# Performance work log

Hardware: AMD Instinct MI355X
Metric: run time of the kernel (lower is better)

Reference implementation:

```python
import jax, jax.numpy as jnp
import numpy as np

B, N, IN_C, HID_C, OUT_C = 64, 1024, 16, 64, 32


def process_graph(graph):
    # graph: [B, N, N]; add self-loops, then row-normalize by inverse degree.
    n = graph.shape[-1]
    g = graph + jnp.eye(n, dtype=graph.dtype)
    deg = jnp.sum(g, axis=-1)                      # [B, N]
    inv_deg = jnp.where(deg == 0, jnp.zeros_like(deg), 1.0 / deg)
    # diag(inv_deg) @ g == row-wise broadcast scale (avoids O(N^3) diag matmul)
    return g * inv_deg[..., None]                  # [B, N, N]


def setup_inputs() -> dict:
    key = jax.random.key(0)
    kx, kg, k1, kb1, k2, kb2 = jax.random.split(key, 6)
    x = jax.random.normal(kx, (B, N, IN_C), dtype=jnp.float32)
    graph = jax.random.uniform(kg, (B, N, N), dtype=jnp.float32)
    # nn.Linear default init: U(-1/sqrt(fan_in), 1/sqrt(fan_in))
    lim1 = 1.0 / np.sqrt(IN_C)
    W1 = jax.random.uniform(k1, (HID_C, IN_C), minval=-lim1, maxval=lim1, dtype=jnp.float32)
    b1 = jax.random.uniform(kb1, (HID_C,), minval=-lim1, maxval=lim1, dtype=jnp.float32)
    lim2 = 1.0 / np.sqrt(HID_C)
    W2 = jax.random.uniform(k2, (OUT_C, HID_C), minval=-lim2, maxval=lim2, dtype=jnp.float32)
    b2 = jax.random.uniform(kb2, (OUT_C,), minval=-lim2, maxval=lim2, dtype=jnp.float32)
    return {"x": x, "graph": graph, "W1": W1, "b1": b1, "W2": W2, "b2": b2}


def reference(x, graph, W1, b1, W2, b2):
    g = process_graph(graph)                                   # [B, N, N]
    h = jnp.einsum('bnc,hc->bnh', x, W1) + b1                  # linear_1
    h = jax.nn.relu(jnp.einsum('bnm,bmh->bnh', g, h))          # propagate + ReLU
    o = jnp.einsum('bnh,oh->bno', h, W2) + b2                  # linear_2
    o = jax.nn.relu(jnp.einsum('bnm,bmo->bno', g, o))          # propagate + ReLU
    return o                                                   # [B, N, OUT_C]
```

## Files before the change

### kernel.cpp

```cpp
#include <hip/hip_runtime.h>

typedef __attribute__((ext_vector_type(8))) short s16x8;
typedef __attribute__((ext_vector_type(8))) unsigned short u16x8;
typedef __attribute__((ext_vector_type(4))) float f32x4;

#define B_   64
#define N_   1024
#define CIN_ 16
#define CH_  64
#define CO_  32

__device__ __forceinline__ unsigned short f2bf(float f){
  unsigned int u = __float_as_uint(f);
  u += 0x7fffu + ((u >> 16) & 1u);
  return (unsigned short)(u >> 16);
}

__global__ __launch_bounds__(256) void k_linear1(
    const float* __restrict__ x, const float* __restrict__ W1,
    const float* __restrict__ b1, unsigned short* __restrict__ H1T){
  int gt   = blockIdx.x * 256 + threadIdx.x;
  int wave = gt >> 6;
  int lane = gt & 63;
  int b    = wave >> 4;
  int nl0  = (wave & 15) << 6;

  const f32x4* xv = (const f32x4*)(x + ((size_t)(b * N_ + nl0 + lane)) * CIN_);
  float xr[16];
#pragma unroll
  for (int i = 0; i < 4; ++i){
    f32x4 v = xv[i];
#pragma unroll
    for (int e = 0; e < 4; ++e) xr[i*4+e] = v[e];
  }
  for (int h = 0; h < CH_; ++h){
    float acc = b1[h];
#pragma unroll
    for (int c = 0; c < CIN_; ++c) acc += xr[c] * W1[h * CIN_ + c];
    H1T[((size_t)(b * CH_ + h)) * N_ + nl0 + lane] = f2bf(acc);
  }
}

__global__ __launch_bounds__(256) void k_prop1(
    const float* __restrict__ graph, const unsigned short* __restrict__ H1T,
    const float* __restrict__ W2, const float* __restrict__ b2,
    unsigned short* __restrict__ O1T){
  __shared__ unsigned short sH2[4][16 * 64];

  const int b    = blockIdx.x >> 4;
  const int m0   = (blockIdx.x & 15) << 6;
  const int tid  = threadIdx.x;
  const int w    = tid >> 6, lane = tid & 63;
  const int l15  = lane & 15, lk = lane >> 4;
  const int gn   = m0 + (w << 4) + l15;
  const int ksd  = (m0 + (w << 4)) >> 5;

  const float* gA = graph + ((size_t)b << 20) + ((size_t)gn << 10) + (lk << 3);
  const unsigned short* hB = H1T + (size_t)(b * CH_ + l15) * N_ + (lk << 3);

  f32x4 acc[4] = {{0,0,0,0},{0,0,0,0},{0,0,0,0},{0,0,0,0}};
  float deg = 0.f;

  f32x4 a0 = __builtin_nontemporal_load((const f32x4*)(gA));
  f32x4 a1 = __builtin_nontemporal_load((const f32x4*)(gA + 4));
  u16x8 b0 = *(const u16x8*)(hB);
  u16x8 b1f = *(const u16x8*)(hB + 16 * N_);
  u16x8 b2f = *(const u16x8*)(hB + 32 * N_);
  u16x8 b3f = *(const u16x8*)(hB + 48 * N_);

  for (int ks = 0; ks < 32; ++ks){
    const int kn = (((ks + 1) & 31) << 5);
    f32x4 na0 = __builtin_nontemporal_load((const f32x4*)(gA + kn));
    f32x4 na1 = __builtin_nontemporal_load((const f32x4*)(gA + kn + 4));
    u16x8 nb0 = *(const u16x8*)(hB + kn);
    u16x8 nb1 = *(const u16x8*)(hB + 16 * N_ + kn);
    u16x8 nb2 = *(const u16x8*)(hB + 32 * N_ + kn);
    u16x8 nb3 = *(const u16x8*)(hB + 48 * N_ + kn);

    float va[8] = {a0[0], a0[1], a0[2], a0[3], a1[0], a1[1], a1[2], a1[3]};
    if (ks == ksd){
      const int d0 = (ks << 5) + (lk << 3);
#pragma unroll
      for (int e = 0; e < 8; ++e) va[e] += (d0 + e == gn) ? 1.f : 0.f;
    }
#pragma unroll
    for (int e = 0; e < 8; ++e) deg += va[e];
    s16x8 af;
#pragma unroll
    for (int e = 0; e < 8; ++e) af[e] = (short)f2bf(va[e]);

    acc[0] = __builtin_amdgcn_mfma_f32_16x16x32_bf16(af, (s16x8)b0,  acc[0], 0, 0, 0);
    acc[1] = __builtin_amdgcn_mfma_f32_16x16x32_bf16(af, (s16x8)b1f, acc[1], 0, 0, 0);
    acc[2] = __builtin_amdgcn_mfma_f32_16x16x32_bf16(af, (s16x8)b2f, acc[2], 0, 0, 0);
    acc[3] = __builtin_amdgcn_mfma_f32_16x16x32_bf16(af, (s16x8)b3f, acc[3], 0, 0, 0);

    a0 = na0; a1 = na1; b0 = nb0; b1f = nb1; b2f = nb2; b3f = nb3;
  }

  deg += __shfl_xor(deg, 16);
  deg += __shfl_xor(deg, 32);
  float ideg = 1.f / deg;
  float idv[4];
#pragma unroll
  for (int j = 0; j < 4; ++j) idv[j] = __shfl(ideg, (lk << 2) + j);

#pragma unroll
  for (int cf = 0; cf < 4; ++cf){
#pragma unroll
    for (int j = 0; j < 4; ++j){
      float hv = acc[cf][j] * idv[j];
      hv = hv > 0.f ? hv : 0.f;
      int row = (lk << 2) + j;
      int col = (cf << 4) + l15;
      sH2[w][(row << 6) + (col ^ ((row & 7) << 3))] = f2bf(hv);
    }
  }
  __syncthreads();
  s16x8 a2[2];
#pragma unroll
  for (int kk = 0; kk < 2; ++kk)
    a2[kk] = *(const s16x8*)&sH2[w][(l15 << 6) + (((kk << 5) + (lk << 3)) ^ ((l15 & 7) << 3))];

  f32x4 acc2[2] = {{0,0,0,0},{0,0,0,0}};
#pragma unroll
  for (int kk = 0; kk < 2; ++kk){
#pragma unroll
    for (int cf = 0; cf < 2; ++cf){
      const f32x4* wp = (const f32x4*)(W2 + ((cf << 4) + l15) * CH_ + (kk << 5) + (lk << 3));
      f32x4 w0 = wp[0], w1 = wp[1];
      s16x8 bw;
#pragma unroll
      for (int e = 0; e < 4; ++e){ bw[e] = (short)f2bf(w0[e]); bw[4 + e] = (short)f2bf(w1[e]); }
      acc2[cf] = __builtin_amdgcn_mfma_f32_16x16x32_bf16(a2[kk], bw, acc2[cf], 0, 0, 0);
    }
  }
#pragma unroll
  for (int cf = 0; cf < 2; ++cf){
    float badd = b2[(cf << 4) + l15];
#pragma unroll
    for (int j = 0; j < 4; ++j){
      float v = acc2[cf][j] + badd;
      int n = m0 + (w << 4) + (lk << 2) + j;
      O1T[((size_t)(b * CO_ + (cf << 4) + l15)) * N_ + n] = f2bf(v);
    }
  }
}

__global__ __launch_bounds__(256) void k_prop2(
    const float* __restrict__ graph, const unsigned short* __restrict__ O1T,
    float* __restrict__ out){
  const int b    = blockIdx.x >> 4;
  const int m0   = (blockIdx.x & 15) << 6;
  const int tid  = threadIdx.x;
  const int w    = tid >> 6, lane = tid & 63;
  const int l15  = lane & 15, lk = lane >> 4;
  const int gn   = m0 + (w << 4) + l15;
  const int ksd  = (m0 + (w << 4)) >> 5;

  const float* gA = graph + ((size_t)b << 20) + ((size_t)gn << 10) + (lk << 3);
  const unsigned short* oB = O1T + (size_t)(b * CO_ + l15) * N_ + (lk << 3);

  f32x4 acc[2] = {{0,0,0,0},{0,0,0,0}};
  float deg = 0.f;

  f32x4 a0 = __builtin_nontemporal_load((const f32x4*)(gA));
  f32x4 a1 = __builtin_nontemporal_load((const f32x4*)(gA + 4));
  u16x8 b0 = *(const u16x8*)(oB);
  u16x8 b1f = *(const u16x8*)(oB + 16 * N_);

  for (int ks = 0; ks < 32; ++ks){
    const int kn = (((ks + 1) & 31) << 5);
    f32x4 na0 = __builtin_nontemporal_load((const f32x4*)(gA + kn));
    f32x4 na1 = __builtin_nontemporal_load((const f32x4*)(gA + kn + 4));
    u16x8 nb0 = *(const u16x8*)(oB + kn);
    u16x8 nb1 = *(const u16x8*)(oB + 16 * N_ + kn);

    float va[8] = {a0[0], a0[1], a0[2], a0[3], a1[0], a1[1], a1[2], a1[3]};
    if (ks == ksd){
      const int d0 = (ks << 5) + (lk << 3);
#pragma unroll
      for (int e = 0; e < 8; ++e) va[e] += (d0 + e == gn) ? 1.f : 0.f;
    }
#pragma unroll
    for (int e = 0; e < 8; ++e) deg += va[e];
    s16x8 af;
#pragma unroll
    for (int e = 0; e < 8; ++e) af[e] = (short)f2bf(va[e]);

    acc[0] = __builtin_amdgcn_mfma_f32_16x16x32_bf16(af, (s16x8)b0,  acc[0], 0, 0, 0);
    acc[1] = __builtin_amdgcn_mfma_f32_16x16x32_bf16(af, (s16x8)b1f, acc[1], 0, 0, 0);

    a0 = na0; a1 = na1; b0 = nb0; b1f = nb1;
  }

  deg += __shfl_xor(deg, 16);
  deg += __shfl_xor(deg, 32);
  float ideg = 1.f / deg;
  float idv[4];
#pragma unroll
  for (int j = 0; j < 4; ++j) idv[j] = __shfl(ideg, (lk << 2) + j);

#pragma unroll
  for (int cf = 0; cf < 2; ++cf){
#pragma unroll
    for (int j = 0; j < 4; ++j){
      float v = acc[cf][j] * idv[j];
      v = v > 0.f ? v : 0.f;
      int n = m0 + (w << 4) + (lk << 2) + j;
      out[((size_t)(b * N_ + n)) * CO_ + (cf << 4) + l15] = v;
    }
  }
}

extern "C" void kernel_launch(void* const* d_in, const int* in_sizes, int n_in,
                              void* d_out, int out_size, void* d_ws, size_t ws_size,
                              hipStream_t stream){
  (void)in_sizes; (void)n_in; (void)out_size; (void)ws_size;
  const float* x     = (const float*)d_in[0];
  const float* graph = (const float*)d_in[1];
  const float* W1    = (const float*)d_in[2];
  const float* b1    = (const float*)d_in[3];
  const float* W2    = (const float*)d_in[4];
  const float* b2    = (const float*)d_in[5];
  float* out = (float*)d_out;

  unsigned short* H1T = (unsigned short*)d_ws;
  unsigned short* O1T = (unsigned short*)((char*)d_ws + ((size_t)8 << 20));

  k_linear1<<<256, 256, 0, stream>>>(x, W1, b1, H1T);
  k_prop1<<<B_ * 16, 256, 0, stream>>>(graph, H1T, W2, b2, O1T);
  k_prop2<<<B_ * 16, 256, 0, stream>>>(graph, O1T, out);
}
```

Before: 526.5 us.

## Cache bf16 graph and inverse degrees in prop1 for reuse in prop2

The first propagation kernel now writes the bf16-converted graph tile (self-loop included) and the per-row inverse degree to workspace. The second propagation kernel reads this half-size bf16 graph instead of re-reading the fp32 graph, and loads the precomputed inverse degree instead of recomputing it. This is meant to cut the dominant graph traffic in prop2 from 256MB to 128MB. The cost is an extra 128MB write in prop1, a two-deep register prefetch with a reversed k loop in prop2, and reliance on workspace being large enough (about 144MB).

```diff
diff --git a/kernel.cpp b/kernel.cpp
--- a/kernel.cpp
+++ b/kernel.cpp
@@ -44,7 +44,8 @@
 __global__ __launch_bounds__(256) void k_prop1(
     const float* __restrict__ graph, const unsigned short* __restrict__ H1T,
     const float* __restrict__ W2, const float* __restrict__ b2,
-    unsigned short* __restrict__ O1T){
+    unsigned short* __restrict__ O1T, unsigned short* __restrict__ GbT,
+    float* __restrict__ idegw){
   __shared__ unsigned short sH2[4][16 * 64];
 
   const int b    = blockIdx.x >> 4;
@@ -57,6 +58,7 @@
 
   const float* gA = graph + ((size_t)b << 20) + ((size_t)gn << 10) + (lk << 3);
   const unsigned short* hB = H1T + (size_t)(b * CH_ + l15) * N_ + (lk << 3);
+  unsigned short* gW = GbT + ((size_t)b << 20) + ((size_t)gn << 10) + (lk << 3);
 
   f32x4 acc[4] = {{0,0,0,0},{0,0,0,0},{0,0,0,0},{0,0,0,0}};
   float deg = 0.f;
@@ -89,6 +91,8 @@
 #pragma unroll
     for (int e = 0; e < 8; ++e) af[e] = (short)f2bf(va[e]);
 
+    *(s16x8*)(gW + (ks << 5)) = af;
+
     acc[0] = __builtin_amdgcn_mfma_f32_16x16x32_bf16(af, (s16x8)b0,  acc[0], 0, 0, 0);
     acc[1] = __builtin_amdgcn_mfma_f32_16x16x32_bf16(af, (s16x8)b1f, acc[1], 0, 0, 0);
     acc[2] = __builtin_amdgcn_mfma_f32_16x16x32_bf16(af, (s16x8)b2f, acc[2], 0, 0, 0);
@@ -100,6 +104,7 @@
   deg += __shfl_xor(deg, 16);
   deg += __shfl_xor(deg, 32);
   float ideg = 1.f / deg;
+  if (lk == 0) idegw[(b << 10) + gn] = ideg;
   float idv[4];
 #pragma unroll
   for (int j = 0; j < 4; ++j) idv[j] = __shfl(ideg, (lk << 2) + j);
@@ -147,58 +152,42 @@
 }
 
 __global__ __launch_bounds__(256) void k_prop2(
-    const float* __restrict__ graph, const unsigned short* __restrict__ O1T,
-    float* __restrict__ out){
+    const unsigned short* __restrict__ GbT, const unsigned short* __restrict__ O1T,
+    const float* __restrict__ idegw, float* __restrict__ out){
   const int b    = blockIdx.x >> 4;
   const int m0   = (blockIdx.x & 15) << 6;
   const int tid  = threadIdx.x;
   const int w    = tid >> 6, lane = tid & 63;
   const int l15  = lane & 15, lk = lane >> 4;
   const int gn   = m0 + (w << 4) + l15;
-  const int ksd  = (m0 + (w << 4)) >> 5;
-
-  const float* gA = graph + ((size_t)b << 20) + ((size_t)gn << 10) + (lk << 3);
+
+  const unsigned short* gA = GbT + ((size_t)b << 20) + ((size_t)gn << 10) + (lk << 3);
   const unsigned short* oB = O1T + (size_t)(b * CO_ + l15) * N_ + (lk << 3);
 
   f32x4 acc[2] = {{0,0,0,0},{0,0,0,0}};
-  float deg = 0.f;
-
-  f32x4 a0 = __builtin_nontemporal_load((const f32x4*)(gA));
-  f32x4 a1 = __builtin_nontemporal_load((const f32x4*)(gA + 4));
-  u16x8 b0 = *(const u16x8*)(oB);
-  u16x8 b1f = *(const u16x8*)(oB + 16 * N_);
-
-  for (int ks = 0; ks < 32; ++ks){
-    const int kn = (((ks + 1) & 31) << 5);
-    f32x4 na0 = __builtin_nontemporal_load((const f32x4*)(gA + kn));
-    f32x4 na1 = __builtin_nontemporal_load((const f32x4*)(gA + kn + 4));
-    u16x8 nb0 = *(const u16x8*)(oB + kn);
-    u16x8 nb1 = *(const u16x8*)(oB + 16 * N_ + kn);
-
-    float va[8] = {a0[0], a0[1], a0[2], a0[3], a1[0], a1[1], a1[2], a1[3]};
-    if (ks == ksd){
-      const int d0 = (ks << 5) + (lk << 3);
-#pragma unroll
-      for (int e = 0; e < 8; ++e) va[e] += (d0 + e == gn) ? 1.f : 0.f;
-    }
-#pragma unroll
-    for (int e = 0; e < 8; ++e) deg += va[e];
-    s16x8 af;
-#pragma unroll
-    for (int e = 0; e < 8; ++e) af[e] = (short)f2bf(va[e]);
-
-    acc[0] = __builtin_amdgcn_mfma_f32_16x16x32_bf16(af, (s16x8)b0,  acc[0], 0, 0, 0);
-    acc[1] = __builtin_amdgcn_mfma_f32_16x16x32_bf16(af, (s16x8)b1f, acc[1], 0, 0, 0);
-
-    a0 = na0; a1 = na1; b0 = nb0; b1f = nb1;
-  }
-
-  deg += __shfl_xor(deg, 16);
-  deg += __shfl_xor(deg, 32);
-  float ideg = 1.f / deg;
-  float idv[4];
-#pragma unroll
-  for (int j = 0; j < 4; ++j) idv[j] = __shfl(ideg, (lk << 2) + j);
+
+  u16x8 aP0 = *(const u16x8*)(gA + (31 << 5));
+  u16x8 bP0 = *(const u16x8*)(oB + (31 << 5));
+  u16x8 cP0 = *(const u16x8*)(oB + 16 * N_ + (31 << 5));
+  u16x8 aP1 = *(const u16x8*)(gA + (30 << 5));
+  u16x8 bP1 = *(const u16x8*)(oB + (30 << 5));
+  u16x8 cP1 = *(const u16x8*)(oB + 16 * N_ + (30 << 5));
+
+#pragma unroll 4
+  for (int ks = 31; ks >= 0; --ks){
+    const int kn = ((ks + 30) & 31) << 5;
+    u16x8 na = *(const u16x8*)(gA + kn);
+    u16x8 nb = *(const u16x8*)(oB + kn);
+    u16x8 nc = *(const u16x8*)(oB + 16 * N_ + kn);
+
+    acc[0] = __builtin_amdgcn_mfma_f32_16x16x32_bf16((s16x8)aP0, (s16x8)bP0, acc[0], 0, 0, 0);
+    acc[1] = __builtin_amdgcn_mfma_f32_16x16x32_bf16((s16x8)aP0, (s16x8)cP0, acc[1], 0, 0, 0);
+
+    aP0 = aP1; bP0 = bP1; cP0 = cP1;
+    aP1 = na;  bP1 = nb;  cP1 = nc;
+  }
+
+  f32x4 idv = *(const f32x4*)(idegw + (b << 10) + m0 + (w << 4) + (lk << 2));
 
 #pragma unroll
   for (int cf = 0; cf < 2; ++cf){
@@ -226,8 +215,10 @@
 
   unsigned short* H1T = (unsigned short*)d_ws;
   unsigned short* O1T = (unsigned short*)((char*)d_ws + ((size_t)8 << 20));
+  float*        idegw = (float*)((char*)d_ws + ((size_t)12 << 20));
+  unsigned short* GbT = (unsigned short*)((char*)d_ws + ((size_t)16 << 20));
 
   k_linear1<<<256, 256, 0, stream>>>(x, W1, b1, H1T);
-  k_prop1<<<B_ * 16, 256, 0, stream>>>(graph, H1T, W2, b2, O1T);
-  k_prop2<<<B_ * 16, 256, 0, stream>>>(graph, O1T, out);
-}
+  k_prop1<<<B_ * 16, 256, 0, stream>>>(graph, H1T, W2, b2, O1T, GbT, idegw);
+  k_prop2<<<B_ * 16, 256, 0, stream>>>(GbT, O1T, idegw, out);
+}
```

New measurement: 507.3 us. -3.6%, faster.
